# Performance work log

Hardware: AMD Instinct MI355X
Metric: run time of the kernel (lower is better)

## Reference

```python
import math
import jax, jax.numpy as jnp
import numpy as np

CLUSTER_RATIO1 = 0.0625
CLUSTER_RATIO2 = 0.35
K_LAYER1 = 8
K_LAYER2 = 3


def _dpc_knn(x, cluster_num, k, key):
    """Density-peak clustering with KNN density. x: [B,N,C] -> idx_cluster [B,N]."""
    B, N, C = x.shape
    sq = jnp.sum(x * x, axis=-1)  # [B,N]
    d2 = sq[:, :, None] + sq[:, None, :] - 2.0 * jnp.einsum('bnc,bmc->bnm', x, x)
    dist = jnp.sqrt(jnp.maximum(d2, 0.0)) / jnp.sqrt(jnp.asarray(C, x.dtype))  # cdist / C**0.5
    # k nearest (smallest) distances
    neg_dn, _ = jax.lax.top_k(-dist, k)
    dist_nearest = -neg_dn  # [B,N,k]
    density = jnp.exp(-jnp.mean(dist_nearest ** 2, axis=-1))
    density = density + jax.random.uniform(key, density.shape, dtype=density.dtype) * 1e-6
    mask = (density[:, None, :] > density[:, :, None]).astype(x.dtype)  # [B,N,N]
    dist_max = jnp.max(dist.reshape(B, -1), axis=-1)[:, None, None]
    parent_dist = jnp.min(dist * mask + dist_max * (1.0 - mask), axis=-1)  # [B,N]
    score = parent_dist * density
    _, index_down = jax.lax.top_k(score, cluster_num)  # [B,cluster_num] cluster centers
    # assign each token to nearest center
    dm = jnp.take_along_axis(dist, index_down[:, :, None], axis=1)  # [B,cluster_num,N]
    idx_cluster = jnp.argmin(dm, axis=1)  # [B,N]
    bidx = jnp.arange(B)[:, None]
    idx_cluster = idx_cluster.at[bidx, index_down].set(
        jnp.broadcast_to(jnp.arange(cluster_num)[None, :], index_down.shape))
    return idx_cluster


def _merge_tokens(x, idx_cluster, cluster_num):
    """Weighted (uniform) scatter-mean of tokens into clusters. x: [B,N,C]."""
    B, N, C = x.shape
    flat = (idx_cluster + jnp.arange(B)[:, None] * cluster_num).reshape(-1)  # [B*N]
    ones = jnp.ones((B * N,), x.dtype)
    all_w = jax.ops.segment_sum(ones, flat, num_segments=B * cluster_num) + 1e-6
    norm_w = 1.0 / all_w[flat]  # token_weight == 1
    merged = jax.ops.segment_sum(x.reshape(B * N, C) * norm_w[:, None], flat,
                                 num_segments=B * cluster_num)
    return merged.reshape(B, cluster_num, C)


def _group(meta1, meta2, idx_cluster2, score_w, score_b):
    """Reorder [meta2[v]; members of cluster v from meta1] per cluster, scaled by modulation."""
    T, K1, C = meta1.shape
    K2 = meta2.shape[1]
    modu = jax.nn.softmax(meta2.mean(axis=2) @ score_w.T + score_b, axis=-1)  # [T,K2]
    # composite sort key: (cluster_id, 0 for meta2 center, 1+i for meta1 member i) -> stable grouping
    cid = jnp.concatenate([jnp.broadcast_to(jnp.arange(K2)[None, :], (T, K2)),
                           idx_cluster2], axis=1)  # [T,K2+K1]
    pos = jnp.concatenate([jnp.zeros((T, K2), jnp.int32),
                           jnp.broadcast_to(jnp.arange(1, K1 + 1, dtype=jnp.int32)[None, :], (T, K1))],
                          axis=1)
    sort_key = cid * (K1 + 2) + pos
    order = jnp.argsort(sort_key, axis=1)  # stable; keys are unique anyway
    tokens = jnp.concatenate([meta2, meta1], axis=1)  # [T,K2+K1,C]
    sorted_tokens = jnp.take_along_axis(tokens, order[:, :, None], axis=1)
    sorted_cid = jnp.take_along_axis(cid, order, axis=1)
    scale = jnp.take_along_axis(modu, sorted_cid, axis=1)  # [T,K2+K1]
    return sorted_tokens * scale[:, :, None]


def setup_inputs() -> dict:
    key = jax.random.key(0)
    k1, k2, k3 = jax.random.split(key, 3)
    T, N, C = 128, 256, 1408
    vis_embed = jax.random.normal(k1, (T, N, C), dtype=jnp.float32)
    score_w = jax.random.normal(k2, (6, 6), dtype=jnp.float32) * 0.1
    score_b = jax.random.normal(k3, (6,), dtype=jnp.float32) * 0.1
    return {"vis_embed": vis_embed, "score_w": score_w, "score_b": score_b}


def reference(vis_embed, score_w, score_b):
    T, N, C = vis_embed.shape
    cn1 = max(math.ceil(N * CLUSTER_RATIO1), 1)      # 16
    cn2 = max(math.ceil(cn1 * CLUSTER_RATIO2), 1)    # 6
    nk = jax.random.split(jax.random.key(42), 2)
    idx1 = _dpc_knn(vis_embed, cn1, K_LAYER1, nk[0])
    meta1 = _merge_tokens(vis_embed, idx1, cn1)       # [T,16,C]
    idx2 = _dpc_knn(meta1, cn2, K_LAYER2, nk[1])
    meta2 = _merge_tokens(meta1, idx2, cn2)           # [T,6,C]
    return _group(meta1, meta2, idx2, score_w, score_b)  # [T,22,C]
```

## Files before the change

### kernel.cpp

```cpp
#include <hip/hip_runtime.h>
#include <math.h>

#define T_BATCH 128
#define N_TOK   256
#define C_DIM   1408
#define CN1     16
#define KNN1    8
#define CN2     6
#define KNN2    3
#define NOUT    22
#define LSTR    40

typedef __attribute__((ext_vector_type(4))) short sh4;
typedef __attribute__((ext_vector_type(8))) short sh8;
typedef __attribute__((ext_vector_type(4))) float f32x4;

union frag_u { sh4 h[2]; sh8 v; };

__device__ inline sh8 ld_frag(const short* p) {
    frag_u u;
    u.h[0] = *(const sh4*)p;
    u.h[1] = *(const sh4*)(p + 4);
    return u.v;
}

struct bf16pair { short hi, lo; };

__device__ inline bf16pair split_bf16(float v) {
    bf16pair r;
    unsigned u = __float_as_uint(v);
    unsigned h = (u + 0x7FFFu + ((u >> 16) & 1u)) >> 16;
    r.hi = (short)h;
    float l = v - __uint_as_float(h << 16);
    unsigned u2 = __float_as_uint(l);
    r.lo = (short)((u2 + 0x7FFFu + ((u2 >> 16) & 1u)) >> 16);
    return r;
}

__global__ __launch_bounds__(256, 2) void gemm_dist_mfma(const float* __restrict__ x,
                                                         float* __restrict__ dist) {
    const int t  = blockIdx.z;
    const int i0 = blockIdx.x * 128;
    const int j0 = blockIdx.y * 128;
    const float* X = x + (size_t)t * N_TOK * C_DIM;

    __shared__ short Ahi[128 * LSTR], Alo[128 * LSTR], Bhi[128 * LSTR], Blo[128 * LSTR];
    __shared__ float nred[512];
    __shared__ float snA[128], snB[128];

    const int tid  = threadIdx.x;
    const int wave = tid >> 6;
    const int lane = tid & 63;
    const int qr   = wave >> 1;
    const int qc   = wave & 1;
    const int srow = tid >> 1;
    const int scol = (tid & 1) * 16;
    const int fr   = lane & 15;
    const int fq   = lane >> 4;

    f32x4 acc[4][4];
#pragma unroll
    for (int a = 0; a < 4; a++)
#pragma unroll
        for (int b = 0; b < 4; b++) acc[a][b] = (f32x4){0.f, 0.f, 0.f, 0.f};

    const float* Arow = X + (size_t)(i0 + srow) * C_DIM + scol;
    const float* Brow = X + (size_t)(j0 + srow) * C_DIM + scol;
    float nA = 0.f, nB = 0.f;

    for (int k0 = 0; k0 < C_DIM; k0 += 32) {
        float av[16], bv[16];
#pragma unroll
        for (int g = 0; g < 4; g++) {
            float4 a = *(const float4*)(Arow + k0 + g * 4);
            float4 b = *(const float4*)(Brow + k0 + g * 4);
            av[g * 4 + 0] = a.x; av[g * 4 + 1] = a.y; av[g * 4 + 2] = a.z; av[g * 4 + 3] = a.w;
            bv[g * 4 + 0] = b.x; bv[g * 4 + 1] = b.y; bv[g * 4 + 2] = b.z; bv[g * 4 + 3] = b.w;
        }
#pragma unroll
        for (int e = 0; e < 16; e++) { nA += av[e] * av[e]; nB += bv[e] * bv[e]; }

        sh4 AH[4], AL[4], BH[4], BL[4];
#pragma unroll
        for (int g = 0; g < 4; g++)
#pragma unroll
            for (int e = 0; e < 4; e++) {
                bf16pair pa = split_bf16(av[g * 4 + e]); AH[g][e] = pa.hi; AL[g][e] = pa.lo;
                bf16pair pb = split_bf16(bv[g * 4 + e]); BH[g][e] = pb.hi; BL[g][e] = pb.lo;
            }
        __syncthreads();
        int so = srow * LSTR + scol;
#pragma unroll
        for (int g = 0; g < 4; g++) {
            *(sh4*)&Ahi[so + g * 4] = AH[g];
            *(sh4*)&Alo[so + g * 4] = AL[g];
            *(sh4*)&Bhi[so + g * 4] = BH[g];
            *(sh4*)&Blo[so + g * 4] = BL[g];
        }
        __syncthreads();

        sh8 fAh[4], fAl[4], fBh[4], fBl[4];
#pragma unroll
        for (int mt = 0; mt < 4; mt++) {
            int ro = (qr * 64 + mt * 16 + fr) * LSTR + fq * 8;
            fAh[mt] = ld_frag(&Ahi[ro]);
            fAl[mt] = ld_frag(&Alo[ro]);
            int co = (qc * 64 + mt * 16 + fr) * LSTR + fq * 8;
            fBh[mt] = ld_frag(&Bhi[co]);
            fBl[mt] = ld_frag(&Blo[co]);
        }
#pragma unroll
        for (int mt = 0; mt < 4; mt++)
#pragma unroll
            for (int nt = 0; nt < 4; nt++) {
                acc[mt][nt] = __builtin_amdgcn_mfma_f32_16x16x32_bf16(fAh[mt], fBh[nt], acc[mt][nt], 0, 0, 0);
                acc[mt][nt] = __builtin_amdgcn_mfma_f32_16x16x32_bf16(fAh[mt], fBl[nt], acc[mt][nt], 0, 0, 0);
                acc[mt][nt] = __builtin_amdgcn_mfma_f32_16x16x32_bf16(fAl[mt], fBh[nt], acc[mt][nt], 0, 0, 0);
            }
    }

    nred[tid] = nA; nred[256 + tid] = nB;
    __syncthreads();
    if (tid < 128) {
        snA[tid] = nred[2 * tid] + nred[2 * tid + 1];
        snB[tid] = nred[256 + 2 * tid] + nred[256 + 2 * tid + 1];
    }
    __syncthreads();

    const float inv_sqrtC = 1.0f / sqrtf((float)C_DIM);
    float* Dt = dist + (size_t)t * N_TOK * N_TOK;
#pragma unroll
    for (int mt = 0; mt < 4; mt++)
#pragma unroll
        for (int nt = 0; nt < 4; nt++) {
            int jl = qc * 64 + nt * 16 + fr;
            float sqj = snB[jl];
            int jg = j0 + jl;
#pragma unroll
            for (int r = 0; r < 4; r++) {
                int il = qr * 64 + mt * 16 + fq * 4 + r;
                int ig = i0 + il;
                float d2 = snA[il] + sqj - 2.0f * acc[mt][nt][r];
                float v = (ig == jg) ? 0.0f : sqrtf(fmaxf(d2, 0.0f)) * inv_sqrtC;
                Dt[(size_t)ig * N_TOK + jg] = v;
            }
        }
}

__global__ __launch_bounds__(64) void density_kernel(const float* __restrict__ dist,
                                                     float* __restrict__ dens,
                                                     unsigned* __restrict__ dmax) {
    const int t    = blockIdx.y;
    const int lane = threadIdx.x;
    const int i    = blockIdx.x * 64 + lane;
    const float* D = dist + (size_t)t * N_TOK * N_TOK;

    float m[KNN1];
#pragma unroll
    for (int q = 0; q < KNN1; q++) m[q] = 3.4e38f;
    float mx = 0.f;

#pragma unroll 8
    for (int j = 0; j < N_TOK; j++) {
        float d = D[(size_t)j * N_TOK + i];
        mx = fmaxf(mx, d);
        float xv = d;
#pragma unroll
        for (int q = 0; q < KNN1; q++) {
            float lo = fminf(m[q], xv);
            xv = fmaxf(m[q], xv);
            m[q] = lo;
        }
    }
    float s2 = 0.f;
#pragma unroll
    for (int q = 0; q < KNN1; q++) s2 += m[q] * m[q];
    dens[t * N_TOK + i] = expf(-s2 / (float)KNN1);

#pragma unroll
    for (int off = 32; off > 0; off >>= 1) mx = fmaxf(mx, __shfl_xor(mx, off));
    if (lane == 0) atomicMax(&dmax[t], __float_as_uint(mx));
}

__global__ __launch_bounds__(64) void score_kernel(const float* __restrict__ dist,
                                                   const float* __restrict__ dens,
                                                   const unsigned* __restrict__ dmax,
                                                   float* __restrict__ score) {
    const int t    = blockIdx.y;
    const int lane = threadIdx.x;
    const int i    = blockIdx.x * 64 + lane;
    const float* D = dist + (size_t)t * N_TOK * N_TOK;

    __shared__ float sd[N_TOK];
#pragma unroll
    for (int u = 0; u < 4; u++) sd[u * 64 + lane] = dens[t * N_TOK + u * 64 + lane];
    __syncthreads();

    float di = sd[i & (N_TOK - 1)];
    di = dens[t * N_TOK + i];
    float pd = __uint_as_float(dmax[t]);
#pragma unroll 8
    for (int j = 0; j < N_TOK; j++) {
        float d = D[(size_t)j * N_TOK + i];
        float dj = sd[j];
        pd = (dj > di) ? fminf(pd, d) : pd;
    }
    score[t * N_TOK + i] = pd * di;
}

__global__ __launch_bounds__(256) void topk_assign_kernel(const float* __restrict__ dist,
                                                          const float* __restrict__ score,
                                                          int* __restrict__ memb,
                                                          int* __restrict__ cntg,
                                                          int* __restrict__ offg) {
    const int t   = blockIdx.x;
    const int tid = threadIdx.x;
    __shared__ unsigned long long wbest[4];
    __shared__ int centers[CN1];
    __shared__ int bks[N_TOK];
    __shared__ int cnt_s[CN1], off_s[CN1];

    float s = score[t * N_TOK + tid];
    unsigned long long key = ((unsigned long long)__float_as_uint(s) << 32)
                           | (unsigned)(65535 - tid);
    for (int k = 0; k < CN1; k++) {
        unsigned long long m = key;
#pragma unroll
        for (int off = 32; off > 0; off >>= 1) {
            unsigned long long o = __shfl_xor(m, off);
            m = (o > m) ? o : m;
        }
        if ((tid & 63) == 0) wbest[tid >> 6] = m;
        __syncthreads();
        unsigned long long b = wbest[0];
#pragma unroll
        for (int w = 1; w < 4; w++) b = (wbest[w] > b) ? wbest[w] : b;
        int idx = 65535 - (int)(b & 0xFFFFull);
        if (tid == 0) centers[k] = idx;
        if (tid == idx) key = 0;
        __syncthreads();
    }

    const float* Dt = dist + (size_t)t * N_TOK * N_TOK;
    float bd = 3.4e38f; int bk = 0;
#pragma unroll
    for (int k = 0; k < CN1; k++) {
        float d = Dt[(size_t)centers[k] * N_TOK + tid];
        if (d < bd) { bd = d; bk = k; }
    }
#pragma unroll
    for (int k = 0; k < CN1; k++) if (tid == centers[k]) bk = k;

    bks[tid] = bk;
    __syncthreads();
    if (tid < CN1) {
        int c = 0;
        for (int j = 0; j < N_TOK; j++) c += (bks[j] == tid);
        cnt_s[tid] = c;
    }
    __syncthreads();
    if (tid == 0) {
        int o = 0;
        for (int q = 0; q < CN1; q++) { off_s[q] = o; o += cnt_s[q]; }
    }
    __syncthreads();
    int rank = 0;
    for (int j = 0; j < tid; j++) rank += (bks[j] == bk);
    memb[t * N_TOK + off_s[bk] + rank] = tid;
    if (tid < CN1) {
        cntg[t * CN1 + tid] = cnt_s[tid];
        offg[t * CN1 + tid] = off_s[tid];
    }
}

__global__ __launch_bounds__(256) void merge1_kernel(const float* __restrict__ x,
                                                     const int* __restrict__ memb,
                                                     const int* __restrict__ cntg,
                                                     const int* __restrict__ offg,
                                                     float* __restrict__ meta1) {
    const int q   = blockIdx.x;
    const int t   = blockIdx.y;
    const int tid = threadIdx.x;
    const int n    = cntg[t * CN1 + q];
    const int base = t * N_TOK + offg[t * CN1 + q];
    const int c0 = tid, c1 = tid + 256;
    const bool act1 = (c1 < C_DIM / 4);

    float a0x = 0.f, a0y = 0.f, a0z = 0.f, a0w = 0.f;
    float a1x = 0.f, a1y = 0.f, a1z = 0.f, a1w = 0.f;
    for (int m = 0; m < n; m++) {
        int row = memb[base + m];
        const float4* xr = (const float4*)(x + ((size_t)t * N_TOK + row) * C_DIM);
        float4 v0 = xr[c0];
        a0x += v0.x; a0y += v0.y; a0z += v0.z; a0w += v0.w;
        if (act1) {
            float4 v1 = xr[c1];
            a1x += v1.x; a1y += v1.y; a1z += v1.z; a1w += v1.w;
        }
    }
    float w = 1.0f / ((float)n + 1e-6f);
    float4* mr = (float4*)(meta1 + ((size_t)t * CN1 + q) * C_DIM);
    float4 o0; o0.x = a0x * w; o0.y = a0y * w; o0.z = a0z * w; o0.w = a0w * w;
    mr[c0] = o0;
    if (act1) {
        float4 o1; o1.x = a1x * w; o1.y = a1y * w; o1.z = a1z * w; o1.w = a1w * w;
        mr[c1] = o1;
    }
}

__global__ __launch_bounds__(256) void layer2_kernel(const float* __restrict__ meta1,
                                                     const float* __restrict__ score_w,
                                                     const float* __restrict__ score_b,
                                                     float* __restrict__ out) {
    const int t   = blockIdx.x;
    const int tid = threadIdx.x;
    const float* M = meta1 + (size_t)t * CN1 * C_DIM;

    __shared__ float buf[CN1][132];
    __shared__ float d2s[CN1][CN1];
    __shared__ float m2[CN2][C_DIM];
    __shared__ float dens[CN1], scor[CN1], nrm[CN1], rmx[CN1];
    __shared__ int   centers[CN2], idx2s[CN1], cnt2[CN2];
    __shared__ float modu[CN2], msum[CN2];
    __shared__ int   srcRow[NOUT], cidArr[NOUT];
    __shared__ float dmax_sh;

    const int ti = tid >> 4;
    const int tj = tid & 15;

    float acc = 0.f;
    for (int c0 = 0; c0 < C_DIM; c0 += 128) {
        for (int e = tid; e < CN1 * 128; e += 256) {
            int r = e >> 7, c = e & 127;
            buf[r][c] = M[(size_t)r * C_DIM + c0 + c];
        }
        __syncthreads();
#pragma unroll
        for (int cc = 0; cc < 128; cc += 4) {
            float4 a = *(const float4*)&buf[ti][cc];
            float4 b = *(const float4*)&buf[tj][cc];
            acc += a.x * b.x + a.y * b.y + a.z * b.z + a.w * b.w;
        }
        __syncthreads();
    }
    if (ti == tj) nrm[ti] = acc;
    __syncthreads();

    const float inv_sqrtC = 1.0f / sqrtf((float)C_DIM);
    {
        float d2 = nrm[ti] + nrm[tj] - 2.f * acc;
        d2s[ti][tj] = sqrtf(fmaxf(d2, 0.f)) * inv_sqrtC;
    }
    __syncthreads();

    if (tid < CN1) {
        float m0 = 3.4e38f, m1 = 3.4e38f, m2v = 3.4e38f, mx = 0.f;
        for (int j = 0; j < CN1; j++) {
            float d = d2s[tid][j];
            mx = fmaxf(mx, d);
            if (d < m2v) {
                m2v = d;
                if (m2v < m1) { float tmp = m2v; m2v = m1; m1 = tmp; }
                if (m1 < m0)  { float tmp = m1;  m1 = m0;  m0 = tmp; }
            }
        }
        dens[tid] = expf(-(m0 * m0 + m1 * m1 + m2v * m2v) / (float)KNN2);
        rmx[tid] = mx;
    }
    __syncthreads();
    if (tid == 0) {
        float g = 0.f;
        for (int j = 0; j < CN1; j++) g = fmaxf(g, rmx[j]);
        dmax_sh = g;
    }
    __syncthreads();

    if (tid < CN1) {
        float di = dens[tid];
        float pd = dmax_sh;
        for (int j = 0; j < CN1; j++)
            if (dens[j] > di) pd = fminf(pd, d2s[tid][j]);
        scor[tid] = pd * di;
    }
    __syncthreads();

    if (tid == 0) {
        for (int k = 0; k < CN2; k++) {
            float best = -3.4e38f; int bi = 0;
            for (int j = 0; j < CN1; j++)
                if (scor[j] > best) { best = scor[j]; bi = j; }
            centers[k] = bi;
            scor[bi] = -3.4e38f;
        }
    }
    __syncthreads();

    if (tid < CN1) {
        float bd = 3.4e38f; int bk = 0;
#pragma unroll
        for (int k = 0; k < CN2; k++) {
            float d = d2s[centers[k]][tid];
            if (d < bd) { bd = d; bk = k; }
        }
#pragma unroll
        for (int k = 0; k < CN2; k++) if (tid == centers[k]) bk = k;
        idx2s[tid] = bk;
    }
    __syncthreads();

    if (tid == 0) {
        for (int v = 0; v < CN2; v++) cnt2[v] = 0;
        for (int i = 0; i < CN1; i++) cnt2[idx2s[i]]++;
        int slot = 0;
        for (int v = 0; v < CN2; v++) {
            srcRow[slot] = CN1 + v; cidArr[slot] = v; slot++;
            for (int i = 0; i < CN1; i++)
                if (idx2s[i] == v) { srcRow[slot] = i; cidArr[slot] = v; slot++; }
        }
        for (int v = 0; v < CN2; v++) msum[v] = 0.f;
    }
    __syncthreads();

    float ls[CN2] = {0.f, 0.f, 0.f, 0.f, 0.f, 0.f};
    for (int ch = tid; ch < C_DIM; ch += 256) {
        float a6[CN2] = {0.f, 0.f, 0.f, 0.f, 0.f, 0.f};
        for (int r = 0; r < CN1; r++) {
            float v = M[(size_t)r * C_DIM + ch];
            int c = idx2s[r];
#pragma unroll
            for (int q = 0; q < CN2; q++) a6[q] += (c == q) ? v : 0.f;
        }
#pragma unroll
        for (int q = 0; q < CN2; q++) {
            float mv = a6[q] / ((float)cnt2[q] + 1e-6f);
            m2[q][ch] = mv;
            ls[q] += mv;
        }
    }
#pragma unroll
    for (int q = 0; q < CN2; q++) atomicAdd(&msum[q], ls[q]);
    __syncthreads();

    if (tid == 0) {
        float mean[CN2], lg[CN2];
        for (int v = 0; v < CN2; v++) mean[v] = msum[v] / (float)C_DIM;
        float mxl = -3.4e38f;
        for (int u = 0; u < CN2; u++) {
            float s = score_b[u];
            for (int v = 0; v < CN2; v++) s += mean[v] * score_w[u * CN2 + v];
            lg[u] = s;
            mxl = fmaxf(mxl, s);
        }
        float den = 0.f;
        for (int u = 0; u < CN2; u++) { lg[u] = expf(lg[u] - mxl); den += lg[u]; }
        for (int u = 0; u < CN2; u++) modu[u] = lg[u] / den;
    }
    __syncthreads();

    float* ob = out + (size_t)t * NOUT * C_DIM;
    for (int ch = tid; ch < C_DIM; ch += 256) {
#pragma unroll
        for (int s = 0; s < NOUT; s++) {
            int r = srcRow[s];
            float v = (r < CN1) ? M[(size_t)r * C_DIM + ch] : m2[r - CN1][ch];
            ob[(size_t)s * C_DIM + ch] = v * modu[cidArr[s]];
        }
    }
}

extern "C" void kernel_launch(void* const* d_in, const int* in_sizes, int n_in,
                              void* d_out, int out_size, void* d_ws, size_t ws_size,
                              hipStream_t stream) {
    const float* x  = (const float*)d_in[0];
    const float* sw = (const float*)d_in[1];
    const float* sb = (const float*)d_in[2];
    float* out = (float*)d_out;

    float* ws     = (float*)d_ws;
    float* dist   = ws;
    float* meta1  = dist + (size_t)T_BATCH * N_TOK * N_TOK;
    float* dens   = meta1 + (size_t)T_BATCH * CN1 * C_DIM;
    float* score  = dens + (size_t)T_BATCH * N_TOK;
    int*   memb   = (int*)(score + (size_t)T_BATCH * N_TOK);
    int*   cntg   = memb + (size_t)T_BATCH * N_TOK;
    int*   offg   = cntg + T_BATCH * CN1;
    unsigned* dmax = (unsigned*)(offg + T_BATCH * CN1);

    (void)hipMemsetAsync(dmax, 0, T_BATCH * sizeof(unsigned), stream);
    gemm_dist_mfma<<<dim3(2, 2, T_BATCH), 256, 0, stream>>>(x, dist);
    density_kernel<<<dim3(4, T_BATCH), 64, 0, stream>>>(dist, dens, dmax);
    score_kernel<<<dim3(4, T_BATCH), 64, 0, stream>>>(dist, dens, dmax, score);
    topk_assign_kernel<<<T_BATCH, 256, 0, stream>>>(dist, score, memb, cntg, offg);
    merge1_kernel<<<dim3(CN1, T_BATCH), 256, 0, stream>>>(x, memb, cntg, offg, meta1);
    layer2_kernel<<<T_BATCH, 256, 0, stream>>>(meta1, sw, sb, out);
}
```

Before: 503.9 us.

## Fuse density/score/topk into one kernel and streamline diagonal-tile GEMM split

Merges the density, score and top-k/assign kernels into one per-batch kernel. The per-batch max becomes a shared-memory reduction, which removes the memset, the atomics and the dens/score round trips through global memory. In the distance GEMM, diagonal tiles reuse the A tile for B, skipping the duplicate loads, splits and LDS stores. The hi part of the bf16 split becomes truncation with packed pair writes, and launch bounds are raised to 3 blocks per CU. Truncating hi changes which bits go into lo but keeps hi+lo precision. The fused kernel uses fewer, larger blocks, so it exposes less parallelism for the density passes.

Result: faster. 487.5 us (-3.3%).

```diff
diff --git a/kernel.cpp b/kernel.cpp
--- a/kernel.cpp
+++ b/kernel.cpp
@@ -24,28 +24,29 @@
     return u.v;
 }
 
-struct bf16pair { short hi, lo; };
-
-__device__ inline bf16pair split_bf16(float v) {
-    bf16pair r;
-    unsigned u = __float_as_uint(v);
-    unsigned h = (u + 0x7FFFu + ((u >> 16) & 1u)) >> 16;
-    r.hi = (short)h;
-    float l = v - __uint_as_float(h << 16);
-    unsigned u2 = __float_as_uint(l);
-    r.lo = (short)((u2 + 0x7FFFu + ((u2 >> 16) & 1u)) >> 16);
-    return r;
-}
-
-__global__ __launch_bounds__(256, 2) void gemm_dist_mfma(const float* __restrict__ x,
+__device__ inline void split2(float v0, float v1, unsigned& hip, unsigned& lop) {
+    unsigned u0 = __float_as_uint(v0);
+    unsigned u1 = __float_as_uint(v1);
+    hip = (u0 >> 16) | (u1 & 0xFFFF0000u);
+    float l0 = v0 - __uint_as_float(u0 & 0xFFFF0000u);
+    float l1 = v1 - __uint_as_float(u1 & 0xFFFF0000u);
+    unsigned w0 = __float_as_uint(l0);
+    unsigned w1 = __float_as_uint(l1);
+    w0 = w0 + 0x7FFFu + ((w0 >> 16) & 1u);
+    w1 = w1 + 0x7FFFu + ((w1 >> 16) & 1u);
+    lop = (w0 >> 16) | (w1 & 0xFFFF0000u);
+}
+
+__global__ __launch_bounds__(256, 3) void gemm_dist_mfma(const float* __restrict__ x,
                                                          float* __restrict__ dist) {
     const int t  = blockIdx.z;
     const int i0 = blockIdx.x * 128;
     const int j0 = blockIdx.y * 128;
+    const bool diag = (i0 == j0);
     const float* X = x + (size_t)t * N_TOK * C_DIM;
 
     __shared__ short Ahi[128 * LSTR], Alo[128 * LSTR], Bhi[128 * LSTR], Blo[128 * LSTR];
-    __shared__ float nred[512];
+    __shared__ float nredA[256], nredB[256];
     __shared__ float snA[128], snB[128];
 
     const int tid  = threadIdx.x;
@@ -58,6 +59,9 @@
     const int fr   = lane & 15;
     const int fq   = lane >> 4;
 
+    const short* BhiS = diag ? Ahi : Bhi;
+    const short* BloS = diag ? Alo : Blo;
+
     f32x4 acc[4][4];
 #pragma unroll
     for (int a = 0; a < 4; a++)
@@ -73,29 +77,37 @@
 #pragma unroll
         for (int g = 0; g < 4; g++) {
             float4 a = *(const float4*)(Arow + k0 + g * 4);
-            float4 b = *(const float4*)(Brow + k0 + g * 4);
             av[g * 4 + 0] = a.x; av[g * 4 + 1] = a.y; av[g * 4 + 2] = a.z; av[g * 4 + 3] = a.w;
-            bv[g * 4 + 0] = b.x; bv[g * 4 + 1] = b.y; bv[g * 4 + 2] = b.z; bv[g * 4 + 3] = b.w;
-        }
-#pragma unroll
-        for (int e = 0; e < 16; e++) { nA += av[e] * av[e]; nB += bv[e] * bv[e]; }
-
-        sh4 AH[4], AL[4], BH[4], BL[4];
-#pragma unroll
-        for (int g = 0; g < 4; g++)
-#pragma unroll
-            for (int e = 0; e < 4; e++) {
-                bf16pair pa = split_bf16(av[g * 4 + e]); AH[g][e] = pa.hi; AL[g][e] = pa.lo;
-                bf16pair pb = split_bf16(bv[g * 4 + e]); BH[g][e] = pb.hi; BL[g][e] = pb.lo;
+        }
+#pragma unroll
+        for (int e = 0; e < 16; e++) nA += av[e] * av[e];
+        if (!diag) {
+#pragma unroll
+            for (int g = 0; g < 4; g++) {
+                float4 b = *(const float4*)(Brow + k0 + g * 4);
+                bv[g * 4 + 0] = b.x; bv[g * 4 + 1] = b.y; bv[g * 4 + 2] = b.z; bv[g * 4 + 3] = b.w;
             }
-        __syncthreads();
-        int so = srow * LSTR + scol;
-#pragma unroll
-        for (int g = 0; g < 4; g++) {
-            *(sh4*)&Ahi[so + g * 4] = AH[g];
-            *(sh4*)&Alo[so + g * 4] = AL[g];
-            *(sh4*)&Bhi[so + g * 4] = BH[g];
-            *(sh4*)&Blo[so + g * 4] = BL[g];
+#pragma unroll
+            for (int e = 0; e < 16; e++) nB += bv[e] * bv[e];
+        }
+
+        unsigned ah[8], al[8], bh[8], bl[8];
+#pragma unroll
+        for (int p = 0; p < 8; p++) split2(av[2 * p], av[2 * p + 1], ah[p], al[p]);
+        if (!diag) {
+#pragma unroll
+            for (int p = 0; p < 8; p++) split2(bv[2 * p], bv[2 * p + 1], bh[p], bl[p]);
+        }
+        __syncthreads();
+        unsigned* AhiW = (unsigned*)&Ahi[srow * LSTR + scol];
+        unsigned* AloW = (unsigned*)&Alo[srow * LSTR + scol];
+#pragma unroll
+        for (int p = 0; p < 8; p++) { AhiW[p] = ah[p]; AloW[p] = al[p]; }
+        if (!diag) {
+            unsigned* BhiW = (unsigned*)&Bhi[srow * LSTR + scol];
+            unsigned* BloW = (unsigned*)&Blo[srow * LSTR + scol];
+#pragma unroll
+            for (int p = 0; p < 8; p++) { BhiW[p] = bh[p]; BloW[p] = bl[p]; }
         }
         __syncthreads();
 
@@ -106,8 +118,8 @@
             fAh[mt] = ld_frag(&Ahi[ro]);
             fAl[mt] = ld_frag(&Alo[ro]);
             int co = (qc * 64 + mt * 16 + fr) * LSTR + fq * 8;
-            fBh[mt] = ld_frag(&Bhi[co]);
-            fBl[mt] = ld_frag(&Blo[co]);
+            fBh[mt] = ld_frag(&BhiS[co]);
+            fBl[mt] = ld_frag(&BloS[co]);
         }
 #pragma unroll
         for (int mt = 0; mt < 4; mt++)
@@ -119,11 +131,12 @@
             }
     }
 
-    nred[tid] = nA; nred[256 + tid] = nB;
+    nredA[tid] = nA;
+    nredB[tid] = diag ? nA : nB;
     __syncthreads();
     if (tid < 128) {
-        snA[tid] = nred[2 * tid] + nred[2 * tid + 1];
-        snB[tid] = nred[256 + 2 * tid] + nred[256 + 2 * tid + 1];
+        snA[tid] = nredA[2 * tid] + nredA[2 * tid + 1];
+        snB[tid] = nredB[2 * tid] + nredB[2 * tid + 1];
     }
     __syncthreads();
 
@@ -147,22 +160,28 @@
         }
 }
 
-__global__ __launch_bounds__(64) void density_kernel(const float* __restrict__ dist,
-                                                     float* __restrict__ dens,
-                                                     unsigned* __restrict__ dmax) {
-    const int t    = blockIdx.y;
-    const int lane = threadIdx.x;
-    const int i    = blockIdx.x * 64 + lane;
+__global__ __launch_bounds__(256) void dpc1_fused(const float* __restrict__ dist,
+                                                  int* __restrict__ memb,
+                                                  int* __restrict__ cntg,
+                                                  int* __restrict__ offg) {
+    const int t   = blockIdx.x;
+    const int tid = threadIdx.x;
     const float* D = dist + (size_t)t * N_TOK * N_TOK;
+
+    __shared__ float dens_s[N_TOK];
+    __shared__ float red[N_TOK];
+    __shared__ unsigned long long wbest[4];
+    __shared__ int centers[CN1];
+    __shared__ int bks[N_TOK];
+    __shared__ int cnt_s[CN1], off_s[CN1];
 
     float m[KNN1];
 #pragma unroll
     for (int q = 0; q < KNN1; q++) m[q] = 3.4e38f;
     float mx = 0.f;
-
 #pragma unroll 8
     for (int j = 0; j < N_TOK; j++) {
-        float d = D[(size_t)j * N_TOK + i];
+        float d = D[(size_t)j * N_TOK + tid];
         mx = fmaxf(mx, d);
         float xv = d;
 #pragma unroll
@@ -175,62 +194,36 @@
     float s2 = 0.f;
 #pragma unroll
     for (int q = 0; q < KNN1; q++) s2 += m[q] * m[q];
-    dens[t * N_TOK + i] = expf(-s2 / (float)KNN1);
-
-#pragma unroll
-    for (int off = 32; off > 0; off >>= 1) mx = fmaxf(mx, __shfl_xor(mx, off));
-    if (lane == 0) atomicMax(&dmax[t], __float_as_uint(mx));
-}
-
-__global__ __launch_bounds__(64) void score_kernel(const float* __restrict__ dist,
-                                                   const float* __restrict__ dens,
-                                                   const unsigned* __restrict__ dmax,
-                                                   float* __restrict__ score) {
-    const int t    = blockIdx.y;
-    const int lane = threadIdx.x;
-    const int i    = blockIdx.x * 64 + lane;
-    const float* D = dist + (size_t)t * N_TOK * N_TOK;
-
-    __shared__ float sd[N_TOK];
-#pragma unroll
-    for (int u = 0; u < 4; u++) sd[u * 64 + lane] = dens[t * N_TOK + u * 64 + lane];
-    __syncthreads();
-
-    float di = sd[i & (N_TOK - 1)];
-    di = dens[t * N_TOK + i];
-    float pd = __uint_as_float(dmax[t]);
+    float dens = expf(-s2 / (float)KNN1);
+    dens_s[tid] = dens;
+    red[tid] = mx;
+    __syncthreads();
+#pragma unroll
+    for (int s = 128; s > 0; s >>= 1) {
+        if (tid < s) red[tid] = fmaxf(red[tid], red[tid + s]);
+        __syncthreads();
+    }
+    float dmax = red[0];
+
+    float pd = dmax;
 #pragma unroll 8
     for (int j = 0; j < N_TOK; j++) {
-        float d = D[(size_t)j * N_TOK + i];
-        float dj = sd[j];
-        pd = (dj > di) ? fminf(pd, d) : pd;
-    }
-    score[t * N_TOK + i] = pd * di;
-}
-
-__global__ __launch_bounds__(256) void topk_assign_kernel(const float* __restrict__ dist,
-                                                          const float* __restrict__ score,
-                                                          int* __restrict__ memb,
-                                                          int* __restrict__ cntg,
-                                                          int* __restrict__ offg) {
-    const int t   = blockIdx.x;
-    const int tid = threadIdx.x;
-    __shared__ unsigned long long wbest[4];
-    __shared__ int centers[CN1];
-    __shared__ int bks[N_TOK];
-    __shared__ int cnt_s[CN1], off_s[CN1];
-
-    float s = score[t * N_TOK + tid];
-    unsigned long long key = ((unsigned long long)__float_as_uint(s) << 32)
+        float d = D[(size_t)j * N_TOK + tid];
+        float dj = dens_s[j];
+        pd = (dj > dens) ? fminf(pd, d) : pd;
+    }
+    float score = pd * dens;
+
+    unsigned long long key = ((unsigned long long)__float_as_uint(score) << 32)
                            | (unsigned)(65535 - tid);
     for (int k = 0; k < CN1; k++) {
-        unsigned long long m = key;
+        unsigned long long mm = key;
 #pragma unroll
         for (int off = 32; off > 0; off >>= 1) {
-            unsigned long long o = __shfl_xor(m, off);
-            m = (o > m) ? o : m;
-        }
-        if ((tid & 63) == 0) wbest[tid >> 6] = m;
+            unsigned long long o = __shfl_xor(mm, off);
+            mm = (o > mm) ? o : mm;
+        }
+        if ((tid & 63) == 0) wbest[tid >> 6] = mm;
         __syncthreads();
         unsigned long long b = wbest[0];
 #pragma unroll
@@ -241,11 +234,10 @@
         __syncthreads();
     }
 
-    const float* Dt = dist + (size_t)t * N_TOK * N_TOK;
     float bd = 3.4e38f; int bk = 0;
 #pragma unroll
     for (int k = 0; k < CN1; k++) {
-        float d = Dt[(size_t)centers[k] * N_TOK + tid];
+        float d = D[(size_t)centers[k] * N_TOK + tid];
         if (d < bd) { bd = d; bk = k; }
     }
 #pragma unroll
@@ -479,18 +471,12 @@
     float* ws     = (float*)d_ws;
     float* dist   = ws;
     float* meta1  = dist + (size_t)T_BATCH * N_TOK * N_TOK;
-    float* dens   = meta1 + (size_t)T_BATCH * CN1 * C_DIM;
-    float* score  = dens + (size_t)T_BATCH * N_TOK;
-    int*   memb   = (int*)(score + (size_t)T_BATCH * N_TOK);
+    int*   memb   = (int*)(meta1 + (size_t)T_BATCH * CN1 * C_DIM);
     int*   cntg   = memb + (size_t)T_BATCH * N_TOK;
     int*   offg   = cntg + T_BATCH * CN1;
-    unsigned* dmax = (unsigned*)(offg + T_BATCH * CN1);
-
-    (void)hipMemsetAsync(dmax, 0, T_BATCH * sizeof(unsigned), stream);
+
     gemm_dist_mfma<<<dim3(2, 2, T_BATCH), 256, 0, stream>>>(x, dist);
-    density_kernel<<<dim3(4, T_BATCH), 64, 0, stream>>>(dist, dens, dmax);
-    score_kernel<<<dim3(4, T_BATCH), 64, 0, stream>>>(dist, dens, dmax, score);
-    topk_assign_kernel<<<T_BATCH, 256, 0, stream>>>(dist, score, memb, cntg, offg);
+    dpc1_fused<<<T_BATCH, 256, 0, stream>>>(dist, memb, cntg, offg);
     merge1_kernel<<<dim3(CN1, T_BATCH), 256, 0, stream>>>(x, memb, cntg, offg, meta1);
     layer2_kernel<<<T_BATCH, 256, 0, stream>>>(meta1, sw, sb, out);
 }
```
